# Kernel tuning notes

Measured on AMD Instinct MI355X. Metric: run time of the kernel, lower is better.

## Reference

```python
import jax, jax.numpy as jnp
import numpy as np

N_CAPS1 = 32 * 6 * 6   # 1152
CAPS1_DIM = 8
CAPS2_N = 10
CAPS2_DIM = 16
EPS = 1e-07


def squash(s, axis=-1, epsilon=EPS):
    sq = jnp.sum(jnp.square(s), axis=axis, keepdims=True)
    safe_norm = jnp.sqrt(sq + epsilon)
    return (sq / (1.0 + sq)) * (s / safe_norm)


def setup_inputs() -> dict:
    key = jax.random.key(0)
    k1, k2 = jax.random.split(key)
    inputs = jax.random.normal(k1, (512, N_CAPS1 * CAPS1_DIM), dtype=jnp.float32)
    W = jax.random.normal(k2, (1, N_CAPS1, CAPS2_N, CAPS2_DIM, CAPS1_DIM), dtype=jnp.float32) * 0.1
    return {"inputs": inputs, "W": W}


def reference(inputs, W):
    b = inputs.shape[0]
    x = inputs.reshape(b, N_CAPS1, CAPS1_DIM)            # [B, 1152, 8]
    pc = squash(x)                                        # [B, 1152, 8]
    # Fused broadcasted batched matmul (no tiling of W or pc):
    # W[0]: [n, j, d, k]; pc: [b, n, k] -> u_hat: [b, n, j, d]
    u_hat = jnp.einsum('njdk,bnk->bnjd', W[0], pc)
    return u_hat[..., None]                               # [B, 1152, 10, 16, 1]
```

## Files before the change

### kernel.cpp

```cpp
#include <hip/hip_runtime.h>

#define NCAPS 1152
#define KD 8
#define JD 10
#define DD 16
#define BATCH 512
#define BTILE 64

typedef float f32x4 __attribute__((ext_vector_type(4)));

__global__ __launch_bounds__(320) void caps_kernel(
    const float* __restrict__ x,
    const float* __restrict__ W,
    float* __restrict__ out)
{
    const int n  = blockIdx.x;
    const int bb = blockIdx.y;
    const int t  = threadIdx.x;

    __shared__ float pcs[BTILE][KD];

    if (t < BTILE) {
        int b = bb * BTILE + t;
        const float* xp = x + (size_t)b * (NCAPS * KD) + n * KD;
        float4 v0 = *(const float4*)(xp);
        float4 v1 = *(const float4*)(xp + 4);
        float sq = v0.x * v0.x + v0.y * v0.y + v0.z * v0.z + v0.w * v0.w
                 + v1.x * v1.x + v1.y * v1.y + v1.z * v1.z + v1.w * v1.w;
        float scale = sq / ((1.0f + sq) * sqrtf(sq + 1e-7f));
        pcs[t][0] = v0.x * scale;
        pcs[t][1] = v0.y * scale;
        pcs[t][2] = v0.z * scale;
        pcs[t][3] = v0.w * scale;
        pcs[t][4] = v1.x * scale;
        pcs[t][5] = v1.y * scale;
        pcs[t][6] = v1.z * scale;
        pcs[t][7] = v1.w * scale;
    }

    const int c  = t % 40;
    const int g  = t / 40;
    const int j  = c >> 2;
    const int dq = c & 3;
    const float* wp = W + (size_t)n * (JD * DD * KD) + j * (DD * KD) + dq * 4 * KD;
    float4 wA0 = *(const float4*)(wp + 0);
    float4 wB0 = *(const float4*)(wp + 4);
    float4 wA1 = *(const float4*)(wp + 8);
    float4 wB1 = *(const float4*)(wp + 12);
    float4 wA2 = *(const float4*)(wp + 16);
    float4 wB2 = *(const float4*)(wp + 20);
    float4 wA3 = *(const float4*)(wp + 24);
    float4 wB3 = *(const float4*)(wp + 28);

    __syncthreads();

    #pragma unroll
    for (int i = 0; i < 8; ++i) {
        int bl = g * 8 + i;
        float4 p0 = *(const float4*)&pcs[bl][0];
        float4 p1 = *(const float4*)&pcs[bl][4];

        f32x4 acc;
        acc.x = wA0.x*p0.x + wA0.y*p0.y + wA0.z*p0.z + wA0.w*p0.w
              + wB0.x*p1.x + wB0.y*p1.y + wB0.z*p1.z + wB0.w*p1.w;
        acc.y = wA1.x*p0.x + wA1.y*p0.y + wA1.z*p0.z + wA1.w*p0.w
              + wB1.x*p1.x + wB1.y*p1.y + wB1.z*p1.z + wB1.w*p1.w;
        acc.z = wA2.x*p0.x + wA2.y*p0.y + wA2.z*p0.z + wA2.w*p0.w
              + wB2.x*p1.x + wB2.y*p1.y + wB2.z*p1.z + wB2.w*p1.w;
        acc.w = wA3.x*p0.x + wA3.y*p0.y + wA3.z*p0.z + wA3.w*p0.w
              + wB3.x*p1.x + wB3.y*p1.y + wB3.z*p1.z + wB3.w*p1.w;

        int b = bb * BTILE + bl;
        size_t off = (((size_t)b * NCAPS + n) * JD + j) * DD + (dq << 2);
        __builtin_nontemporal_store(acc, (f32x4*)(out + off));
    }
}

extern "C" void kernel_launch(void* const* d_in, const int* in_sizes, int n_in,
                              void* d_out, int out_size, void* d_ws, size_t ws_size,
                              hipStream_t stream) {
    const float* x = (const float*)d_in[0];
    const float* W = (const float*)d_in[1];
    float* out = (float*)d_out;
    dim3 grid(NCAPS, BATCH / BTILE);
    caps_kernel<<<grid, 320, 0, stream>>>(x, W, out);
}
```

Before: 73.68 us.

## Retile blocks over eight capsules by 32 batches for contiguous output rows

Each block now covers 8 consecutive input capsules and 32 batch rows, where before it covered one capsule and 64 batch rows. A 1D grid replaces the 2D one. Each thread loops over all 32 batch rows, so every iteration the whole block writes one contiguous 5 KB span of the output, and the x loads for the squash step also become contiguous. The aim is better write coalescing on a store-bound kernel. In exchange, each W slice is reused over half as many batch rows, which doubles W reads, and there are fewer, longer blocks.

```diff
diff --git a/kernel.cpp b/kernel.cpp
--- a/kernel.cpp
+++ b/kernel.cpp
@@ -5,7 +5,10 @@
 #define JD 10
 #define DD 16
 #define BATCH 512
-#define BTILE 64
+#define NP 8
+#define BT 32
+#define NQ (NCAPS / NP)
+#define NBB (BATCH / BT)
 
 typedef float f32x4 __attribute__((ext_vector_type(4)));
 
@@ -14,35 +17,36 @@
     const float* __restrict__ W,
     float* __restrict__ out)
 {
-    const int n  = blockIdx.x;
-    const int bb = blockIdx.y;
-    const int t  = threadIdx.x;
+    const int bid = blockIdx.x;
+    const int bb  = bid / NQ;
+    const int nq  = bid - bb * NQ;
+    const int n0  = nq * NP;
+    const int b0  = bb * BT;
+    const int t   = threadIdx.x;
 
-    __shared__ float pcs[BTILE][KD];
+    __shared__ float pcs[NP][BT][KD];
 
-    if (t < BTILE) {
-        int b = bb * BTILE + t;
-        const float* xp = x + (size_t)b * (NCAPS * KD) + n * KD;
+    if (t < BT * NP) {
+        int n_l = t & 7;
+        int b_l = t >> 3;
+        const float* xp = x + (size_t)(b0 + b_l) * (NCAPS * KD) + (n0 + n_l) * KD;
         float4 v0 = *(const float4*)(xp);
         float4 v1 = *(const float4*)(xp + 4);
         float sq = v0.x * v0.x + v0.y * v0.y + v0.z * v0.z + v0.w * v0.w
                  + v1.x * v1.x + v1.y * v1.y + v1.z * v1.z + v1.w * v1.w;
         float scale = sq / ((1.0f + sq) * sqrtf(sq + 1e-7f));
-        pcs[t][0] = v0.x * scale;
-        pcs[t][1] = v0.y * scale;
-        pcs[t][2] = v0.z * scale;
-        pcs[t][3] = v0.w * scale;
-        pcs[t][4] = v1.x * scale;
-        pcs[t][5] = v1.y * scale;
-        pcs[t][6] = v1.z * scale;
-        pcs[t][7] = v1.w * scale;
+        float* pp = &pcs[n_l][b_l][0];
+        pp[0] = v0.x * scale;  pp[1] = v0.y * scale;
+        pp[2] = v0.z * scale;  pp[3] = v0.w * scale;
+        pp[4] = v1.x * scale;  pp[5] = v1.y * scale;
+        pp[6] = v1.z * scale;  pp[7] = v1.w * scale;
     }
 
-    const int c  = t % 40;
-    const int g  = t / 40;
-    const int j  = c >> 2;
-    const int dq = c & 3;
-    const float* wp = W + (size_t)n * (JD * DD * KD) + j * (DD * KD) + dq * 4 * KD;
+    const int n_l = t / 40;
+    const int c2  = t - n_l * 40;
+    const int j   = c2 >> 2;
+    const int dq  = c2 & 3;
+    const float* wp = W + (size_t)(n0 + n_l) * (JD * DD * KD) + j * (DD * KD) + dq * 4 * KD;
     float4 wA0 = *(const float4*)(wp + 0);
     float4 wB0 = *(const float4*)(wp + 4);
     float4 wA1 = *(const float4*)(wp + 8);
@@ -54,11 +58,12 @@
 
     __syncthreads();
 
-    #pragma unroll
-    for (int i = 0; i < 8; ++i) {
-        int bl = g * 8 + i;
-        float4 p0 = *(const float4*)&pcs[bl][0];
-        float4 p1 = *(const float4*)&pcs[bl][4];
+    const float* pbase = &pcs[n_l][0][0];
+    size_t rowbase = (size_t)b0 * (NCAPS * JD * DD) + (size_t)n0 * (JD * DD) + 4 * t;
+    #pragma unroll 8
+    for (int b_l = 0; b_l < BT; ++b_l) {
+        float4 p0 = *(const float4*)(pbase + b_l * KD);
+        float4 p1 = *(const float4*)(pbase + b_l * KD + 4);
 
         f32x4 acc;
         acc.x = wA0.x*p0.x + wA0.y*p0.y + wA0.z*p0.z + wA0.w*p0.w
@@ -70,9 +75,7 @@
         acc.w = wA3.x*p0.x + wA3.y*p0.y + wA3.z*p0.z + wA3.w*p0.w
               + wB3.x*p1.x + wB3.y*p1.y + wB3.z*p1.z + wB3.w*p1.w;
 
-        int b = bb * BTILE + bl;
-        size_t off = (((size_t)b * NCAPS + n) * JD + j) * DD + (dq << 2);
-        __builtin_nontemporal_store(acc, (f32x4*)(out + off));
+        __builtin_nontemporal_store(acc, (f32x4*)(out + rowbase + (size_t)b_l * (NCAPS * JD * DD)));
     }
 }
 
@@ -82,6 +85,5 @@
     const float* x = (const float*)d_in[0];
     const float* W = (const float*)d_in[1];
     float* out = (float*)d_out;
-    dim3 grid(NCAPS, BATCH / BTILE);
-    caps_kernel<<<grid, 320, 0, stream>>>(x, W, out);
+    caps_kernel<<<NQ * NBB, 320, 0, stream>>>(x, W, out);
 }
```

After: 78.74 us. 6.9% more time.
